# Kernel tuning notes

Hardware: AMD Instinct MI355X
Metric: run time of the kernel (lower is better)

## Reference

```python
import jax, jax.numpy as jnp
import numpy as np

H = W = 224
NOISE_STD = 0.45
BRIGHTNESS = 1.1          # uniform(0.8, 1.2) in original
ANGLE_DEG = 10.0          # randint(-20, 21) in original
CROP_I, CROP_J, CROP_SZ = 32, 32, 160

# Perspective: startpoints (input corners) -> endpoints (output corners).
STARTPOINTS = [[0, 0], [223, 0], [223, 223], [0, 223]]
ENDPOINTS = [[30, 20], [200, 25], [210, 200], [15, 190]]  # fixed draws within original ranges

def _perspective_coeffs(startpoints, endpoints):
    # Solve homography mapping OUTPUT coords (endpoints) -> INPUT coords (startpoints),
    # same convention as torchvision._get_perspective_coeffs(endpoints, startpoints).
    A = np.zeros((8, 8), dtype=np.float64)
    b = np.zeros((8,), dtype=np.float64)
    for k, ((xi, yi), (xo, yo)) in enumerate(zip(startpoints, endpoints)):
        A[2 * k] = [xo, yo, 1, 0, 0, 0, -xo * xi, -yo * xi]
        b[2 * k] = xi
        A[2 * k + 1] = [0, 0, 0, xo, yo, 1, -xo * yi, -yo * yi]
        b[2 * k + 1] = yi
    return np.linalg.solve(A, b)  # a,b,c,d,e,f,g,h

COEFFS = _perspective_coeffs(STARTPOINTS, ENDPOINTS)

def bilinear_sample(img, src_x, src_y):
    # img: [B,C,H,W]; src_x/src_y: [Ho,Wo] source pixel coords; zero fill outside.
    Hh, Ww = img.shape[-2], img.shape[-1]
    x0 = jnp.floor(src_x); y0 = jnp.floor(src_y)
    wx1 = src_x - x0; wx0 = 1.0 - wx1
    wy1 = src_y - y0; wy0 = 1.0 - wy1
    def gather(yi, xi):
        valid = (xi >= 0) & (xi <= Ww - 1) & (yi >= 0) & (yi <= Hh - 1)
        xc = jnp.clip(xi, 0, Ww - 1).astype(jnp.int32)
        yc = jnp.clip(yi, 0, Hh - 1).astype(jnp.int32)
        return img[:, :, yc, xc] * valid.astype(img.dtype)
    return (gather(y0, x0) * (wy0 * wx0) + gather(y0, x0 + 1) * (wy0 * wx1)
            + gather(y0 + 1, x0) * (wy1 * wx0) + gather(y0 + 1, x0 + 1) * (wy1 * wx1))

def perspective_grid():
    a, b_, c, d, e, f, g, h = [float(v) for v in COEFFS]
    yo, xo = jnp.meshgrid(jnp.arange(H, dtype=jnp.float32), jnp.arange(W, dtype=jnp.float32), indexing='ij')
    denom = g * xo + h * yo + 1.0
    return (a * xo + b_ * yo + c) / denom, (d * xo + e * yo + f) / denom

def rotate_grid(angle_deg):
    cx, cy = (W - 1) / 2.0, (H - 1) / 2.0
    t = jnp.float32(np.deg2rad(angle_deg))
    cos, sin = jnp.cos(t), jnp.sin(t)
    yo, xo = jnp.meshgrid(jnp.arange(H, dtype=jnp.float32), jnp.arange(W, dtype=jnp.float32), indexing='ij')
    dx, dy = xo - cx, yo - cy
    return cx + cos * dx + sin * dy, cy - sin * dx + cos * dy

def setup_inputs() -> dict:
    key = jax.random.key(0)
    k1, k2 = jax.random.split(key)
    x = jax.random.uniform(k1, (128, 3, H, W), dtype=jnp.float32)
    noise = jax.random.normal(k2, (128, 3, H, W), dtype=jnp.float32)
    return {"x": x, "noise": noise}

def reference(x, noise):
    # (hflip result discarded in the original -> no-op)
    x = x + NOISE_STD * noise                       # additive gaussian noise
    x = jnp.clip(x * BRIGHTNESS, 0.0, 1.0)          # adjust_brightness (float clamp to [0,1])
    px, py = perspective_grid()
    x = bilinear_sample(x, px, py)                  # perspective warp, bilinear, fill 0
    rx, ry = rotate_grid(ANGLE_DEG)
    x = bilinear_sample(x, rx, ry)                  # rotate, bilinear, fill 0
    x = x[..., CROP_I:CROP_I + CROP_SZ, CROP_J:CROP_J + CROP_SZ]  # 160x160 crop
    B, C = x.shape[0], x.shape[1]
    x = jax.image.resize(x, (B, C, H, W), method='bicubic')       # bicubic upsample back to 224
    return x
```

## Files before the change

kernel.cpp:

```cpp
#include <hip/hip_runtime.h>
#include <cmath>
#include <cstring>

#define HH 224
#define WW 224
#define CROP 160
#define CI 32
#define CJ 32
#define NCH 384
#define CH_STRIDE (HH*WW)
#define CROP_STRIDE (CROP*CROP)

#define TILE2 32
#define NTIL2 5
#define GCH2 8
#define BH2 64
#define BHCAP 62
#define NG2 18
#define BWSTR 80

#define TILE 16
#define NTIL 10
#define GCH 8
#define BMAXH 33
#define BMAXW 35
#define LROWS 35
#define LSTR  37
#define LWORDS (LROWS*LSTR)

struct AugParams {
  float a, b, c, d, e, f, g, h;
  float cosT, sinT;
};

__device__ __forceinline__ void axis_weights(int o, float w[4], int id[4]) {
  float s = (o + 0.5f) * (160.0f / 224.0f) - 0.5f;
  int base = (int)floorf(s) - 1;
  float sum = 0.0f;
#pragma unroll
  for (int t = 0; t < 4; ++t) {
    int ii = base + t;
    float dd = fabsf(s - (float)ii);
    float kw;
    if (dd < 1.0f)      kw = ((1.5f * dd - 2.5f) * dd) * dd + 1.0f;
    else if (dd < 2.0f) kw = ((-0.5f * dd + 2.5f) * dd - 4.0f) * dd + 2.0f;
    else                kw = 0.0f;
    if (ii < 0 || ii > CROP - 1) kw = 0.0f;
    w[t] = kw;
    sum += kw;
    id[t] = min(max(ii, 0), CROP - 1);
  }
  float inv = 1.0f / sum;
#pragma unroll
  for (int t = 0; t < 4; ++t) w[t] *= inv;
}

__global__ void table_kernel(float4* __restrict__ wt, int4* __restrict__ it) {
  int o = blockIdx.x * blockDim.x + threadIdx.x;
  if (o >= HH) return;
  float w[4]; int id[4];
  axis_weights(o, w, id);
  wt[o] = make_float4(w[0], w[1], w[2], w[3]);
  it[o] = make_int4(id[0], id[1], id[2], id[3]);
}

__device__ __forceinline__ float preproc(float v, float nv) {
  float p = (v + 0.45f * nv) * 1.1f;
  return fminf(fmaxf(p, 0.0f), 1.0f);
}

__device__ __forceinline__ float bf2f(unsigned short u) {
  return __uint_as_float(((unsigned int)u) << 16);
}

__device__ __forceinline__ unsigned short f2bf(float f) {
  unsigned int b = __float_as_uint(f);
  return (unsigned short)((b + 0x7fff + ((b >> 16) & 1)) >> 16);
}

__global__ __launch_bounds__(256) void preproc_kernel(
    const float4* __restrict__ xin, const float4* __restrict__ nin,
    ushort4* __restrict__ pre) {
  int t = blockIdx.x * 256 + threadIdx.x;
  int b = t * 4;
  float4 x0 = xin[b + 0], x1 = xin[b + 1], x2 = xin[b + 2], x3 = xin[b + 3];
  float4 n0 = nin[b + 0], n1 = nin[b + 1], n2 = nin[b + 2], n3 = nin[b + 3];
  ushort4 o0, o1, o2, o3;
  o0.x = f2bf(preproc(x0.x, n0.x)); o0.y = f2bf(preproc(x0.y, n0.y));
  o0.z = f2bf(preproc(x0.z, n0.z)); o0.w = f2bf(preproc(x0.w, n0.w));
  o1.x = f2bf(preproc(x1.x, n1.x)); o1.y = f2bf(preproc(x1.y, n1.y));
  o1.z = f2bf(preproc(x1.z, n1.z)); o1.w = f2bf(preproc(x1.w, n1.w));
  o2.x = f2bf(preproc(x2.x, n2.x)); o2.y = f2bf(preproc(x2.y, n2.y));
  o2.z = f2bf(preproc(x2.z, n2.z)); o2.w = f2bf(preproc(x2.w, n2.w));
  o3.x = f2bf(preproc(x3.x, n3.x)); o3.y = f2bf(preproc(x3.y, n3.y));
  o3.z = f2bf(preproc(x3.z, n3.z)); o3.w = f2bf(preproc(x3.w, n3.w));
  pre[b + 0] = o0; pre[b + 1] = o1; pre[b + 2] = o2; pre[b + 3] = o3;
}

__device__ __forceinline__ void make_taps(int i, int j, const AugParams P,
                                          int txs[16], int tys[16], float wts[16]) {
  const float cx = (WW - 1) * 0.5f, cy = (HH - 1) * 0.5f;
  float xr = (float)(j + CJ), yr = (float)(i + CI);
  float dx = xr - cx, dy = yr - cy;
  float rx = cx + P.cosT * dx + P.sinT * dy;
  float ry = cy - P.sinT * dx + P.cosT * dy;
  float x0f = floorf(rx), y0f = floorf(ry);
  int x0 = (int)x0f, y0 = (int)y0f;
  float wx1 = rx - x0f, wy1 = ry - y0f;
  float rwx[2] = {1.0f - wx1, wx1};
  float rwy[2] = {1.0f - wy1, wy1};
  int k = 0;
#pragma unroll
  for (int ny = 0; ny < 2; ++ny) {
#pragma unroll
    for (int nx = 0; nx < 2; ++nx) {
      int yn = y0 + ny, xn = x0 + nx;
      bool vn = (xn >= 0 && xn <= WW - 1 && yn >= 0 && yn <= HH - 1);
      float wn = rwy[ny] * rwx[nx] * (vn ? 1.0f : 0.0f);
      float xo = (float)xn, yo = (float)yn;
      float inv = 1.0f / (P.g * xo + P.h * yo + 1.0f);
      float px = (P.a * xo + P.b * yo + P.c) * inv;
      float py = (P.d * xo + P.e * yo + P.f) * inv;
      float px0f = floorf(px), py0f = floorf(py);
      int px0 = (int)px0f, py0 = (int)py0f;
      float pwx1 = px - px0f, pwy1 = py - py0f;
      float pwx[2] = {1.0f - pwx1, pwx1};
      float pwy[2] = {1.0f - pwy1, pwy1};
#pragma unroll
      for (int ty = 0; ty < 2; ++ty) {
#pragma unroll
        for (int tx = 0; tx < 2; ++tx) {
          int yt = py0 + ty, xt = px0 + tx;
          bool vt = (xt >= 0 && xt <= WW - 1 && yt >= 0 && yt <= HH - 1);
          tys[k] = min(max(yt, 0), HH - 1);
          txs[k] = min(max(xt, 0), WW - 1);
          wts[k] = wn * pwy[ty] * pwx[tx] * (vt ? 1.0f : 0.0f);
          ++k;
        }
      }
    }
  }
}

__device__ __forceinline__ void make_patches2(int i, int j, const AugParams P,
                                              int by0, int bx0e,
                                              int pofs[4], float wts[16]) {
  const float cx = (WW - 1) * 0.5f, cy = (HH - 1) * 0.5f;
  float xr = (float)(j + CJ), yr = (float)(i + CI);
  float dx = xr - cx, dy = yr - cy;
  float rx = cx + P.cosT * dx + P.sinT * dy;
  float ry = cy - P.sinT * dx + P.cosT * dy;
  float x0f = floorf(rx), y0f = floorf(ry);
  int x0 = (int)x0f, y0 = (int)y0f;
  float wx1 = rx - x0f, wy1 = ry - y0f;
  float rwx[2] = {1.0f - wx1, wx1};
  float rwy[2] = {1.0f - wy1, wy1};
  int n = 0;
#pragma unroll
  for (int ny = 0; ny < 2; ++ny) {
#pragma unroll
    for (int nx = 0; nx < 2; ++nx) {
      int yn = y0 + ny, xn = x0 + nx;
      bool vn = (xn >= 0 && xn <= WW - 1 && yn >= 0 && yn <= HH - 1);
      float wn = rwy[ny] * rwx[nx] * (vn ? 1.0f : 0.0f);
      float xo = (float)xn, yo = (float)yn;
      float inv = 1.0f / (P.g * xo + P.h * yo + 1.0f);
      float px = (P.a * xo + P.b * yo + P.c) * inv;
      float py = (P.d * xo + P.e * yo + P.f) * inv;
      float px0f = floorf(px), py0f = floorf(py);
      int px0 = (int)px0f, py0 = (int)py0f;
      float pwx1 = px - px0f, pwy1 = py - py0f;
      float pwx[2] = {1.0f - pwx1, pwx1};
      float pwy[2] = {1.0f - pwy1, pwy1};
#pragma unroll
      for (int ty = 0; ty < 2; ++ty) {
#pragma unroll
        for (int tx = 0; tx < 2; ++tx) {
          int yt = py0 + ty, xt = px0 + tx;
          bool vt = (xt >= 0 && xt <= WW - 1 && yt >= 0 && yt <= HH - 1);
          wts[n * 4 + ty * 2 + tx] = wn * pwy[ty] * pwx[tx] * (vt ? 1.0f : 0.0f);
        }
      }
      int r0 = py0 - by0 + 1;
      int c0 = px0 - bx0e + 4;
      r0 = min(max(r0, 0), BH2 - 2);
      c0 = min(max(c0, 0), BWSTR - 2);
      pofs[n] = r0 * BWSTR + c0;
      ++n;
    }
  }
}

__global__ __launch_bounds__(256, 3) void warp_pre_kernel(
    const unsigned short* __restrict__ pre, float* __restrict__ crop,
    AugParams P) {
  __shared__ float s_img[2][BH2 * BWSTR];
  int tile = blockIdx.x;
  int ch0  = blockIdx.y * GCH2;
  int i0 = (tile / NTIL2) * TILE2;
  int j0 = (tile % NTIL2) * TILE2;

  const float cx = (WW - 1) * 0.5f, cy = (HH - 1) * 0.5f;
  float rxmin = 1e30f, rxmax = -1e30f, rymin = 1e30f, rymax = -1e30f;
#pragma unroll
  for (int c = 0; c < 4; ++c) {
    float xr = (float)(j0 + CJ + ((c & 1) ? TILE2 - 1 : 0));
    float yr = (float)(i0 + CI + ((c & 2) ? TILE2 - 1 : 0));
    float dx = xr - cx, dy = yr - cy;
    float rx = cx + P.cosT * dx + P.sinT * dy;
    float ry = cy - P.sinT * dx + P.cosT * dy;
    rxmin = fminf(rxmin, rx); rxmax = fmaxf(rxmax, rx);
    rymin = fminf(rymin, ry); rymax = fmaxf(rymax, ry);
  }
  float xnlo = floorf(rxmin), xnhi = floorf(rxmax) + 1.0f;
  float ynlo = floorf(rymin), ynhi = floorf(rymax) + 1.0f;
  float pxmin = 1e30f, pxmax = -1e30f, pymin = 1e30f, pymax = -1e30f;
#pragma unroll
  for (int c = 0; c < 4; ++c) {
    float xo = (c & 1) ? xnhi : xnlo;
    float yo = (c & 2) ? ynhi : ynlo;
    float inv = 1.0f / (P.g * xo + P.h * yo + 1.0f);
    float px = (P.a * xo + P.b * yo + P.c) * inv;
    float py = (P.d * xo + P.e * yo + P.f) * inv;
    pxmin = fminf(pxmin, px); pxmax = fmaxf(pxmax, px);
    pymin = fminf(pymin, py); pymax = fmaxf(pymax, py);
  }
  int bx0 = max(0, (int)floorf(pxmin));
  int bx1 = min(WW - 1, (int)floorf(pxmax) + 1);
  int by0 = max(0, (int)floorf(pymin));
  int by1 = min(HH - 1, (int)floorf(pymax) + 1);
  int bx0e = bx0 & ~3;
  int bh = by1 - by0 + 1;
  int gmax = (bx1 - bx0e + 4) >> 2;
  bool use_lds = (bh <= BHCAP) && (gmax <= NG2 - 1);

  int tid = threadIdx.x;

  if (use_lds) {
    int pofs[4][4]; float wts[4][16];
#pragma unroll
    for (int k = 0; k < 4; ++k) {
      int p = tid + k * 256;
      make_patches2(i0 + (p >> 5), j0 + (p & 31), P, by0, bx0e, pofs[k], wts[k]);
    }

    for (int s = tid; s < 2 * BH2 * BWSTR; s += 256)
      ((float*)s_img)[s] = 0.0f;
    __syncthreads();

    int nslots = bh * NG2;
    {
      const unsigned short* pb = pre + (size_t)ch0 * CH_STRIDE;
#pragma unroll
      for (int q = 0; q < 5; ++q) {
        int s = tid + q * 256;
        if (s < nslots) {
          int r = s / NG2, g = s - r * NG2;
          int x = bx0e - 4 + g * 4;
          if (x >= 0 && g <= gmax) {
            ushort4 v = *(const ushort4*)(pb + (by0 + r) * WW + x);
            *(float4*)&s_img[0][(r + 1) * BWSTR + g * 4] =
                make_float4(bf2f(v.x), bf2f(v.y), bf2f(v.z), bf2f(v.w));
          }
        }
      }
      __syncthreads();
    }

    int buf = 0;
    for (int cc = 0; cc < GCH2; ++cc) {
      int ch = ch0 + cc;
      bool more = (cc < GCH2 - 1);
      ushort4 xv[5];
      if (more) {
        const unsigned short* pb = pre + (size_t)(ch + 1) * CH_STRIDE;
#pragma unroll
        for (int q = 0; q < 5; ++q) {
          int s = tid + q * 256;
          if (s < nslots) {
            int r = s / NG2, g = s - r * NG2;
            int x = bx0e - 4 + g * 4;
            if (x >= 0 && g <= gmax)
              xv[q] = *(const ushort4*)(pb + (by0 + r) * WW + x);
          }
        }
      }
      const float* sb = s_img[buf];
      float* cb = crop + (size_t)ch * CROP_STRIDE;
#pragma unroll
      for (int k = 0; k < 4; ++k) {
        int p = tid + k * 256;
        float acc = 0.0f;
#pragma unroll
        for (int n = 0; n < 4; ++n) {
          int o = pofs[k][n];
          float v00 = sb[o],         v01 = sb[o + 1];
          float v10 = sb[o + BWSTR], v11 = sb[o + BWSTR + 1];
          acc = fmaf(wts[k][n * 4 + 0], v00, acc);
          acc = fmaf(wts[k][n * 4 + 1], v01, acc);
          acc = fmaf(wts[k][n * 4 + 2], v10, acc);
          acc = fmaf(wts[k][n * 4 + 3], v11, acc);
        }
        cb[i0 * CROP + (p >> 5) * CROP + j0 + (p & 31)] = acc;
      }
      if (more) {
        float* sw = s_img[buf ^ 1];
#pragma unroll
        for (int q = 0; q < 5; ++q) {
          int s = tid + q * 256;
          if (s < nslots) {
            int r = s / NG2, g = s - r * NG2;
            int x = bx0e - 4 + g * 4;
            if (x >= 0 && g <= gmax) {
              *(float4*)&sw[(r + 1) * BWSTR + g * 4] =
                  make_float4(bf2f(xv[q].x), bf2f(xv[q].y),
                              bf2f(xv[q].z), bf2f(xv[q].w));
            }
          }
        }
      }
      __syncthreads();
      buf ^= 1;
    }
  } else {
    for (int k = 0; k < 4; ++k) {
      int p = tid + k * 256;
      int i = i0 + (p >> 5), j = j0 + (p & 31);
      int txs[16], tys[16]; float w[16];
      make_taps(i, j, P, txs, tys, w);
      for (int cc = 0; cc < GCH2; ++cc) {
        int ch = ch0 + cc;
        const unsigned short* pb = pre + (size_t)ch * CH_STRIDE;
        float acc = 0.0f;
#pragma unroll
        for (int t = 0; t < 16; ++t)
          acc = fmaf(w[t], bf2f(pb[tys[t] * WW + txs[t]]), acc);
        crop[(size_t)ch * CROP_STRIDE + i * CROP + j] = acc;
      }
    }
  }
}

__device__ __forceinline__ void make_patches(int i, int j, const AugParams P,
                                             int by0, int bx0, int bh, int bw,
                                             int pofs[4], float wts[16]) {
  const float cx = (WW - 1) * 0.5f, cy = (HH - 1) * 0.5f;
  float xr = (float)(j + CJ), yr = (float)(i + CI);
  float dx = xr - cx, dy = yr - cy;
  float rx = cx + P.cosT * dx + P.sinT * dy;
  float ry = cy - P.sinT * dx + P.cosT * dy;
  float x0f = floorf(rx), y0f = floorf(ry);
  int x0 = (int)x0f, y0 = (int)y0f;
  float wx1 = rx - x0f, wy1 = ry - y0f;
  float rwx[2] = {1.0f - wx1, wx1};
  float rwy[2] = {1.0f - wy1, wy1};
  int n = 0;
#pragma unroll
  for (int ny = 0; ny < 2; ++ny) {
#pragma unroll
    for (int nx = 0; nx < 2; ++nx) {
      int yn = y0 + ny, xn = x0 + nx;
      bool vn = (xn >= 0 && xn <= WW - 1 && yn >= 0 && yn <= HH - 1);
      float wn = rwy[ny] * rwx[nx] * (vn ? 1.0f : 0.0f);
      float xo = (float)xn, yo = (float)yn;
      float inv = 1.0f / (P.g * xo + P.h * yo + 1.0f);
      float px = (P.a * xo + P.b * yo + P.c) * inv;
      float py = (P.d * xo + P.e * yo + P.f) * inv;
      float px0f = floorf(px), py0f = floorf(py);
      int px0 = (int)px0f, py0 = (int)py0f;
      float pwx1 = px - px0f, pwy1 = py - py0f;
      float pwx[2] = {1.0f - pwx1, pwx1};
      float pwy[2] = {1.0f - pwy1, pwy1};
#pragma unroll
      for (int ty = 0; ty < 2; ++ty) {
#pragma unroll
        for (int tx = 0; tx < 2; ++tx) {
          int yt = py0 + ty, xt = px0 + tx;
          bool vt = (xt >= 0 && xt <= WW - 1 && yt >= 0 && yt <= HH - 1);
          wts[n * 4 + ty * 2 + tx] = wn * pwy[ty] * pwx[tx] * (vt ? 1.0f : 0.0f);
        }
      }
      int ly = py0 - by0;
      int lx = px0 - bx0;
      if (ly < -1 || ly > bh - 1) ly = 0;
      if (lx < -1 || lx > bw - 1) lx = 0;
      pofs[n] = (ly + 1) * LSTR + (lx + 1);
      ++n;
    }
  }
}

__global__ __launch_bounds__(256) void warp_direct_kernel(
    const float* __restrict__ xin, const float* __restrict__ nin,
    float* __restrict__ crop, AugParams P) {
  __shared__ float s_img[2][LWORDS];
  int tile = blockIdx.x;
  int ch0  = blockIdx.y * GCH;
  int i0 = (tile / NTIL) * TILE;
  int j0 = (tile % NTIL) * TILE;

  const float cx = (WW - 1) * 0.5f, cy = (HH - 1) * 0.5f;
  float rxmin = 1e30f, rxmax = -1e30f, rymin = 1e30f, rymax = -1e30f;
#pragma unroll
  for (int c = 0; c < 4; ++c) {
    float xr = (float)(j0 + CJ + ((c & 1) ? TILE - 1 : 0));
    float yr = (float)(i0 + CI + ((c & 2) ? TILE - 1 : 0));
    float dx = xr - cx, dy = yr - cy;
    float rx = cx + P.cosT * dx + P.sinT * dy;
    float ry = cy - P.sinT * dx + P.cosT * dy;
    rxmin = fminf(rxmin, rx); rxmax = fmaxf(rxmax, rx);
    rymin = fminf(rymin, ry); rymax = fmaxf(rymax, ry);
  }
  float xnlo = floorf(rxmin), xnhi = floorf(rxmax) + 1.0f;
  float ynlo = floorf(rymin), ynhi = floorf(rymax) + 1.0f;
  float pxmin = 1e30f, pxmax = -1e30f, pymin = 1e30f, pymax = -1e30f;
#pragma unroll
  for (int c = 0; c < 4; ++c) {
    float xo = (c & 1) ? xnhi : xnlo;
    float yo = (c & 2) ? ynhi : ynlo;
    float inv = 1.0f / (P.g * xo + P.h * yo + 1.0f);
    float px = (P.a * xo + P.b * yo + P.c) * inv;
    float py = (P.d * xo + P.e * yo + P.f) * inv;
    pxmin = fminf(pxmin, px); pxmax = fmaxf(pxmax, px);
    pymin = fminf(pymin, py); pymax = fmaxf(pymax, py);
  }
  int bx0 = max(0, (int)floorf(pxmin));
  int bx1 = min(WW - 1, (int)floorf(pxmax) + 1);
  int by0 = max(0, (int)floorf(pymin));
  int by1 = min(HH - 1, (int)floorf(pymax) + 1);
  int bw = bx1 - bx0 + 1;
  int bh = by1 - by0 + 1;
  bool use_lds = (bw <= BMAXW && bh <= BMAXH);

  int tid = threadIdx.x;
  int i = i0 + (tid >> 4);
  int j = j0 + (tid & 15);
  int opix = i * CROP + j;

  if (use_lds) {
    int pofs[4]; float wts[16];
    make_patches(i, j, P, by0, bx0, bh, bw, pofs, wts);
    for (int s = tid; s < 2 * LWORDS; s += 256)
      ((float*)s_img)[s] = 0.0f;
    __syncthreads();
    {
      const float* xb = xin + (size_t)ch0 * CH_STRIDE;
      const float* nb = nin + (size_t)ch0 * CH_STRIDE;
      int r = tid >> 5, c = tid & 31;
#pragma unroll
      for (int rr = 0; rr < 5; ++rr) {
        int rcur = r + rr * 8;
        if (rcur < bh && c < bw) {
          int g = (by0 + rcur) * WW + bx0 + c;
          s_img[0][(rcur + 1) * LSTR + (c + 1)] = preproc(xb[g], nb[g]);
        }
      }
      if (bw > 32) {
        int r2 = tid >> 2, c2 = 32 + (tid & 3);
        if (r2 < bh && c2 < bw) {
          int g = (by0 + r2) * WW + bx0 + c2;
          s_img[0][(r2 + 1) * LSTR + (c2 + 1)] = preproc(xb[g], nb[g]);
        }
      }
      __syncthreads();
    }
    int buf = 0;
    int r = tid >> 5, c = tid & 31;
    int r2 = tid >> 2, c2 = 32 + (tid & 3);
    for (int cc = 0; cc < GCH; ++cc) {
      int ch = ch0 + cc;
      bool more = (cc < GCH - 1);
      float xv[5], nv[5], xe = 0.0f, ne = 0.0f;
      if (more) {
        const float* xb = xin + (size_t)(ch + 1) * CH_STRIDE;
        const float* nb = nin + (size_t)(ch + 1) * CH_STRIDE;
#pragma unroll
        for (int rr = 0; rr < 5; ++rr) {
          int rcur = r + rr * 8;
          if (rcur < bh && c < bw) {
            int g = (by0 + rcur) * WW + bx0 + c;
            xv[rr] = xb[g]; nv[rr] = nb[g];
          }
        }
        if (bw > 32 && r2 < bh && c2 < bw) {
          int g = (by0 + r2) * WW + bx0 + c2;
          xe = xb[g]; ne = nb[g];
        }
      }
      const float* sb = s_img[buf];
      float acc = 0.0f;
#pragma unroll
      for (int n = 0; n < 4; ++n) {
        int p = pofs[n];
        acc = fmaf(wts[n * 4 + 0], sb[p], acc);
        acc = fmaf(wts[n * 4 + 1], sb[p + 1], acc);
        acc = fmaf(wts[n * 4 + 2], sb[p + LSTR], acc);
        acc = fmaf(wts[n * 4 + 3], sb[p + LSTR + 1], acc);
      }
      crop[(size_t)ch * CROP_STRIDE + opix] = acc;
      if (more) {
        float* sw = s_img[buf ^ 1];
#pragma unroll
        for (int rr = 0; rr < 5; ++rr) {
          int rcur = r + rr * 8;
          if (rcur < bh && c < bw)
            sw[(rcur + 1) * LSTR + (c + 1)] = preproc(xv[rr], nv[rr]);
        }
        if (bw > 32 && r2 < bh && c2 < bw)
          sw[(r2 + 1) * LSTR + (c2 + 1)] = preproc(xe, ne);
      }
      __syncthreads();
      buf ^= 1;
    }
  } else {
    int txs[16], tys[16]; float wts[16];
    make_taps(i, j, P, txs, tys, wts);
    for (int cc = 0; cc < GCH; ++cc) {
      int ch = ch0 + cc;
      const float* xb = xin + (size_t)ch * CH_STRIDE;
      const float* nb = nin + (size_t)ch * CH_STRIDE;
      float acc = 0.0f;
#pragma unroll
      for (int t = 0; t < 16; ++t) {
        int g = tys[t] * WW + txs[t];
        acc = fmaf(wts[t], preproc(xb[g], nb[g]), acc);
      }
      crop[(size_t)ch * CROP_STRIDE + opix] = acc;
    }
  }
}

#define STRIPROWS 28
#define HROWS 25
__global__ __launch_bounds__(256) void resize_strips_kernel(
    const float* __restrict__ crop, const float4* __restrict__ wt,
    const int4* __restrict__ it, float* __restrict__ out) {
  __shared__ float hbuf[HROWS * WW];
  int s = blockIdx.x;
  int ch = blockIdx.y;
  int r0 = max(0, s * 20 - 2);
  const float* cb = crop + (size_t)ch * CROP_STRIDE;
  int tid = threadIdx.x;

  for (int e = tid; e < HROWS * WW; e += 256) {
    int r = e / WW;
    int xo = e - r * WW;
    int cr = min(r0 + r, CROP - 1);
    float4 wx = wt[xo]; int4 ix = it[xo];
    const float* row = cb + cr * CROP;
    hbuf[e] = wx.x * row[ix.x] + wx.y * row[ix.y] +
              wx.z * row[ix.z] + wx.w * row[ix.w];
  }
  __syncthreads();
  for (int e = tid; e < STRIPROWS * WW; e += 256) {
    int yl = e / WW;
    int xo = e - yl * WW;
    int yo = s * STRIPROWS + yl;
    float4 wy = wt[yo]; int4 iy = it[yo];
    float o = wy.x * hbuf[(iy.x - r0) * WW + xo] +
              wy.y * hbuf[(iy.y - r0) * WW + xo] +
              wy.z * hbuf[(iy.z - r0) * WW + xo] +
              wy.w * hbuf[(iy.w - r0) * WW + xo];
    __builtin_nontemporal_store(o, &out[((size_t)ch * HH + yo) * WW + xo]);
  }
}

__device__ float crop_val(const float* __restrict__ xb, const float* __restrict__ nb,
                          int i, int j, AugParams P) {
  int txs[16], tys[16]; float wts[16];
  make_taps(i, j, P, txs, tys, wts);
  float acc = 0.0f;
#pragma unroll
  for (int t = 0; t < 16; ++t)
    acc = fmaf(wts[t], preproc(xb[tys[t] * WW + txs[t]], nb[tys[t] * WW + txs[t]]), acc);
  return acc;
}

__global__ __launch_bounds__(256) void fused_fallback_kernel(
    const float* __restrict__ xin, const float* __restrict__ nin,
    float* __restrict__ out, AugParams P, int total) {
  int stride = gridDim.x * blockDim.x;
  for (int idx = blockIdx.x * blockDim.x + threadIdx.x; idx < total; idx += stride) {
    int xo = idx % WW;
    int t2 = idx / WW;
    int yo = t2 % HH;
    int ch = t2 / HH;
    float wxa[4]; int ixa[4]; axis_weights(xo, wxa, ixa);
    float wya[4]; int iya[4]; axis_weights(yo, wya, iya);
    const float* xb = xin + (size_t)ch * CH_STRIDE;
    const float* nb = nin + (size_t)ch * CH_STRIDE;
    float acc = 0.0f;
#pragma unroll
    for (int ty = 0; ty < 4; ++ty)
#pragma unroll
      for (int tx = 0; tx < 4; ++tx)
        acc += wya[ty] * wxa[tx] * crop_val(xb, nb, iya[ty], ixa[tx], P);
    out[idx] = acc;
  }
}

static void solve_coeffs(double C[8]) {
  const double sp[4][2] = {{0, 0}, {223, 0}, {223, 223}, {0, 223}};
  const double ep[4][2] = {{30, 20}, {200, 25}, {210, 200}, {15, 190}};
  double A[8][9];
  for (int k = 0; k < 4; ++k) {
    double xi = sp[k][0], yi = sp[k][1], xo = ep[k][0], yo = ep[k][1];
    double r0[9] = {xo, yo, 1, 0, 0, 0, -xo * xi, -yo * xi, xi};
    double r1[9] = {0, 0, 0, xo, yo, 1, -xo * yi, -yo * yi, yi};
    std::memcpy(A[2 * k], r0, sizeof r0);
    std::memcpy(A[2 * k + 1], r1, sizeof r1);
  }
  for (int col = 0; col < 8; ++col) {
    int piv = col;
    for (int r = col + 1; r < 8; ++r)
      if (std::fabs(A[r][col]) > std::fabs(A[piv][col])) piv = r;
    if (piv != col)
      for (int cc = 0; cc < 9; ++cc) { double t = A[col][cc]; A[col][cc] = A[piv][cc]; A[piv][cc] = t; }
    double p = A[col][col];
    for (int r = 0; r < 8; ++r) {
      if (r == col) continue;
      double fmul = A[r][col] / p;
      for (int cc = col; cc < 9; ++cc) A[r][cc] -= fmul * A[col][cc];
    }
  }
  for (int r = 0; r < 8; ++r) C[r] = A[r][8] / A[r][r];
}

extern "C" void kernel_launch(void* const* d_in, const int* in_sizes, int n_in,
                              void* d_out, int out_size, void* d_ws, size_t ws_size,
                              hipStream_t stream) {
  const float* xin = (const float*)d_in[0];
  const float* nin = (const float*)d_in[1];
  float* out = (float*)d_out;

  double C[8];
  solve_coeffs(C);
  AugParams P;
  P.a = (float)C[0]; P.b = (float)C[1]; P.c = (float)C[2]; P.d = (float)C[3];
  P.e = (float)C[4]; P.f = (float)C[5]; P.g = (float)C[6]; P.h = (float)C[7];
  double t = 10.0 * M_PI / 180.0;
  P.cosT = (float)std::cos(t);
  P.sinT = (float)std::sin(t);

  const int total = NCH * HH * WW;
  const size_t PRE_BYTES = (size_t)NCH * CH_STRIDE * 2;
  const size_t CROP_BYTES = (size_t)NCH * CROP_STRIDE * 4;

  const size_t TBLW_OFF = PRE_BYTES + 256;
  const size_t TBLI_OFF = TBLW_OFF + 3584;
  const size_t CROPF_OFF = TBLI_OFF + 3584;
  const size_t need_full = CROPF_OFF + CROP_BYTES;
  const size_t need_med = 8192 + CROP_BYTES;

  if (ws_size >= need_full) {
    unsigned short* pre = (unsigned short*)d_ws;
    float4* wt = (float4*)((char*)d_ws + TBLW_OFF);
    int4*   it = (int4*)((char*)d_ws + TBLI_OFF);
    float* crop = (float*)((char*)d_ws + CROPF_OFF);

    hipLaunchKernelGGL(table_kernel, dim3(1), dim3(256), 0, stream, wt, it);
    hipLaunchKernelGGL(preproc_kernel, dim3(total / 16 / 256), dim3(256), 0, stream,
                       (const float4*)xin, (const float4*)nin, (ushort4*)pre);
    dim3 g1(NTIL2 * NTIL2, NCH / GCH2);
    hipLaunchKernelGGL(warp_pre_kernel, g1, dim3(256), 0, stream, pre, crop, P);
    dim3 g2(HH / STRIPROWS, NCH);
    hipLaunchKernelGGL(resize_strips_kernel, g2, dim3(256), 0, stream, crop, wt, it, out);
  } else if (ws_size >= need_med) {
    float4* wt = (float4*)d_ws;
    int4*   it = (int4*)((char*)d_ws + 3584);
    float* crop = (float*)((char*)d_ws + 8192);

    hipLaunchKernelGGL(table_kernel, dim3(1), dim3(256), 0, stream, wt, it);
    dim3 g1(NTIL * NTIL, NCH / GCH);
    hipLaunchKernelGGL(warp_direct_kernel, g1, dim3(256), 0, stream, xin, nin, crop, P);
    dim3 g2(HH / STRIPROWS, NCH);
    hipLaunchKernelGGL(resize_strips_kernel, g2, dim3(256), 0, stream, crop, wt, it, out);
  } else {
    hipLaunchKernelGGL(fused_fallback_kernel, dim3(2048), dim3(256), 0, stream,
                       xin, nin, out, P, total);
  }
}
```

Baseline: 121.0 us.

## Shrink warp LDS tile, swizzle blocks across XCDs, inline resize tables, widen preproc

Several independent changes. The warp kernel's LDS tile shrinks from 64x80 to 46x56 floats so occupancy can rise from 3 to 4 blocks per CU, and it gains a right-edge bound check. The warp and preproc kernels remap block IDs so neighbouring blocks spread across the 8 XCDs. The separate table kernel is removed, and each resize block recomputes its bicubic weights into shared memory, which drops one launch but repeats a little work in every block. Preproc now writes ushort8 vectors, with its loads separated from the conversion by a scheduling barrier. The smaller tile fits fewer source rows, so more tiles may fall back to the slower non-LDS path.

```diff
diff --git a/kernel.cpp b/kernel.cpp
--- a/kernel.cpp
+++ b/kernel.cpp
@@ -14,10 +14,10 @@
 #define TILE2 32
 #define NTIL2 5
 #define GCH2 8
-#define BH2 64
-#define BHCAP 62
-#define NG2 18
-#define BWSTR 80
+#define BROWS 46
+#define BHCAP 44
+#define NG2 14
+#define BSTR 56
 
 #define TILE 16
 #define NTIL 10
@@ -27,6 +27,8 @@
 #define LROWS 35
 #define LSTR  37
 #define LWORDS (LROWS*LSTR)
+
+typedef unsigned short ushort8 __attribute__((ext_vector_type(8)));
 
 struct AugParams {
   float a, b, c, d, e, f, g, h;
@@ -55,15 +57,6 @@
   for (int t = 0; t < 4; ++t) w[t] *= inv;
 }
 
-__global__ void table_kernel(float4* __restrict__ wt, int4* __restrict__ it) {
-  int o = blockIdx.x * blockDim.x + threadIdx.x;
-  if (o >= HH) return;
-  float w[4]; int id[4];
-  axis_weights(o, w, id);
-  wt[o] = make_float4(w[0], w[1], w[2], w[3]);
-  it[o] = make_int4(id[0], id[1], id[2], id[3]);
-}
-
 __device__ __forceinline__ float preproc(float v, float nv) {
   float p = (v + 0.45f * nv) * 1.1f;
   return fminf(fmaxf(p, 0.0f), 1.0f);
@@ -80,21 +73,27 @@
 
 __global__ __launch_bounds__(256) void preproc_kernel(
     const float4* __restrict__ xin, const float4* __restrict__ nin,
-    ushort4* __restrict__ pre) {
-  int t = blockIdx.x * 256 + threadIdx.x;
-  int b = t * 4;
-  float4 x0 = xin[b + 0], x1 = xin[b + 1], x2 = xin[b + 2], x3 = xin[b + 3];
-  float4 n0 = nin[b + 0], n1 = nin[b + 1], n2 = nin[b + 2], n3 = nin[b + 3];
-  ushort4 o0, o1, o2, o3;
-  o0.x = f2bf(preproc(x0.x, n0.x)); o0.y = f2bf(preproc(x0.y, n0.y));
-  o0.z = f2bf(preproc(x0.z, n0.z)); o0.w = f2bf(preproc(x0.w, n0.w));
-  o1.x = f2bf(preproc(x1.x, n1.x)); o1.y = f2bf(preproc(x1.y, n1.y));
-  o1.z = f2bf(preproc(x1.z, n1.z)); o1.w = f2bf(preproc(x1.w, n1.w));
-  o2.x = f2bf(preproc(x2.x, n2.x)); o2.y = f2bf(preproc(x2.y, n2.y));
-  o2.z = f2bf(preproc(x2.z, n2.z)); o2.w = f2bf(preproc(x2.w, n2.w));
-  o3.x = f2bf(preproc(x3.x, n3.x)); o3.y = f2bf(preproc(x3.y, n3.y));
-  o3.z = f2bf(preproc(x3.z, n3.z)); o3.w = f2bf(preproc(x3.w, n3.w));
-  pre[b + 0] = o0; pre[b + 1] = o1; pre[b + 2] = o2; pre[b + 3] = o3;
+    ushort8* __restrict__ pre) {
+  int blk = blockIdx.x;
+  blk = (blk & 7) * 588 + (blk >> 3);
+  int g0 = blk * 512 + threadIdx.x;
+  int g1 = g0 + 256;
+  float4 xa = xin[2 * g0], xb = xin[2 * g0 + 1];
+  float4 xc = xin[2 * g1], xd = xin[2 * g1 + 1];
+  float4 na = nin[2 * g0], nb = nin[2 * g0 + 1];
+  float4 nc = nin[2 * g1], nd = nin[2 * g1 + 1];
+  __builtin_amdgcn_sched_barrier(0);
+  ushort8 oa, ob;
+  oa[0] = f2bf(preproc(xa.x, na.x)); oa[1] = f2bf(preproc(xa.y, na.y));
+  oa[2] = f2bf(preproc(xa.z, na.z)); oa[3] = f2bf(preproc(xa.w, na.w));
+  oa[4] = f2bf(preproc(xb.x, nb.x)); oa[5] = f2bf(preproc(xb.y, nb.y));
+  oa[6] = f2bf(preproc(xb.z, nb.z)); oa[7] = f2bf(preproc(xb.w, nb.w));
+  ob[0] = f2bf(preproc(xc.x, nc.x)); ob[1] = f2bf(preproc(xc.y, nc.y));
+  ob[2] = f2bf(preproc(xc.z, nc.z)); ob[3] = f2bf(preproc(xc.w, nc.w));
+  ob[4] = f2bf(preproc(xd.x, nd.x)); ob[5] = f2bf(preproc(xd.y, nd.y));
+  ob[6] = f2bf(preproc(xd.z, nd.z)); ob[7] = f2bf(preproc(xd.w, nd.w));
+  pre[g0] = oa;
+  pre[g1] = ob;
 }
 
 __device__ __forceinline__ void make_taps(int i, int j, const AugParams P,
@@ -183,20 +182,22 @@
       }
       int r0 = py0 - by0 + 1;
       int c0 = px0 - bx0e + 4;
-      r0 = min(max(r0, 0), BH2 - 2);
-      c0 = min(max(c0, 0), BWSTR - 2);
-      pofs[n] = r0 * BWSTR + c0;
+      r0 = min(max(r0, 0), BROWS - 2);
+      c0 = min(max(c0, 0), BSTR - 2);
+      pofs[n] = r0 * BSTR + c0;
       ++n;
     }
   }
 }
 
-__global__ __launch_bounds__(256, 3) void warp_pre_kernel(
+__global__ __launch_bounds__(256, 4) void warp_pre_kernel(
     const unsigned short* __restrict__ pre, float* __restrict__ crop,
     AugParams P) {
-  __shared__ float s_img[2][BH2 * BWSTR];
-  int tile = blockIdx.x;
-  int ch0  = blockIdx.y * GCH2;
+  __shared__ float s_img[2][BROWS * BSTR];
+  int lb = blockIdx.x + blockIdx.y * (NTIL2 * NTIL2);
+  lb = (lb & 7) * 150 + (lb >> 3);
+  int tile = lb % (NTIL2 * NTIL2);
+  int ch0  = (lb / (NTIL2 * NTIL2)) * GCH2;
   int i0 = (tile / NTIL2) * TILE2;
   int j0 = (tile % NTIL2) * TILE2;
 
@@ -244,7 +245,7 @@
       make_patches2(i0 + (p >> 5), j0 + (p & 31), P, by0, bx0e, pofs[k], wts[k]);
     }
 
-    for (int s = tid; s < 2 * BH2 * BWSTR; s += 256)
+    for (int s = tid; s < 2 * BROWS * BSTR; s += 256)
       ((float*)s_img)[s] = 0.0f;
     __syncthreads();
 
@@ -252,14 +253,14 @@
     {
       const unsigned short* pb = pre + (size_t)ch0 * CH_STRIDE;
 #pragma unroll
-      for (int q = 0; q < 5; ++q) {
+      for (int q = 0; q < 3; ++q) {
         int s = tid + q * 256;
         if (s < nslots) {
           int r = s / NG2, g = s - r * NG2;
           int x = bx0e - 4 + g * 4;
-          if (x >= 0 && g <= gmax) {
+          if (x >= 0 && x <= WW - 4 && g <= gmax) {
             ushort4 v = *(const ushort4*)(pb + (by0 + r) * WW + x);
-            *(float4*)&s_img[0][(r + 1) * BWSTR + g * 4] =
+            *(float4*)&s_img[0][(r + 1) * BSTR + g * 4] =
                 make_float4(bf2f(v.x), bf2f(v.y), bf2f(v.z), bf2f(v.w));
           }
         }
@@ -271,16 +272,16 @@
     for (int cc = 0; cc < GCH2; ++cc) {
       int ch = ch0 + cc;
       bool more = (cc < GCH2 - 1);
-      ushort4 xv[5];
+      ushort4 xv[3];
       if (more) {
         const unsigned short* pb = pre + (size_t)(ch + 1) * CH_STRIDE;
 #pragma unroll
-        for (int q = 0; q < 5; ++q) {
+        for (int q = 0; q < 3; ++q) {
           int s = tid + q * 256;
           if (s < nslots) {
             int r = s / NG2, g = s - r * NG2;
             int x = bx0e - 4 + g * 4;
-            if (x >= 0 && g <= gmax)
+            if (x >= 0 && x <= WW - 4 && g <= gmax)
               xv[q] = *(const ushort4*)(pb + (by0 + r) * WW + x);
           }
         }
@@ -294,8 +295,8 @@
 #pragma unroll
         for (int n = 0; n < 4; ++n) {
           int o = pofs[k][n];
-          float v00 = sb[o],         v01 = sb[o + 1];
-          float v10 = sb[o + BWSTR], v11 = sb[o + BWSTR + 1];
+          float v00 = sb[o],        v01 = sb[o + 1];
+          float v10 = sb[o + BSTR], v11 = sb[o + BSTR + 1];
           acc = fmaf(wts[k][n * 4 + 0], v00, acc);
           acc = fmaf(wts[k][n * 4 + 1], v01, acc);
           acc = fmaf(wts[k][n * 4 + 2], v10, acc);
@@ -306,13 +307,13 @@
       if (more) {
         float* sw = s_img[buf ^ 1];
 #pragma unroll
-        for (int q = 0; q < 5; ++q) {
+        for (int q = 0; q < 3; ++q) {
           int s = tid + q * 256;
           if (s < nslots) {
             int r = s / NG2, g = s - r * NG2;
             int x = bx0e - 4 + g * 4;
-            if (x >= 0 && g <= gmax) {
-              *(float4*)&sw[(r + 1) * BWSTR + g * 4] =
+            if (x >= 0 && x <= WW - 4 && g <= gmax) {
+              *(float4*)&sw[(r + 1) * BSTR + g * 4] =
                   make_float4(bf2f(xv[q].x), bf2f(xv[q].y),
                               bf2f(xv[q].z), bf2f(xv[q].w));
             }
@@ -533,20 +534,29 @@
 #define STRIPROWS 28
 #define HROWS 25
 __global__ __launch_bounds__(256) void resize_strips_kernel(
-    const float* __restrict__ crop, const float4* __restrict__ wt,
-    const int4* __restrict__ it, float* __restrict__ out) {
+    const float* __restrict__ crop, float* __restrict__ out) {
   __shared__ float hbuf[HROWS * WW];
+  __shared__ float4 swt[HH];
+  __shared__ int4 sit[HH];
   int s = blockIdx.x;
   int ch = blockIdx.y;
   int r0 = max(0, s * 20 - 2);
   const float* cb = crop + (size_t)ch * CROP_STRIDE;
   int tid = threadIdx.x;
 
+  if (tid < HH) {
+    float w[4]; int id[4];
+    axis_weights(tid, w, id);
+    swt[tid] = make_float4(w[0], w[1], w[2], w[3]);
+    sit[tid] = make_int4(id[0], id[1], id[2], id[3]);
+  }
+  __syncthreads();
+
   for (int e = tid; e < HROWS * WW; e += 256) {
     int r = e / WW;
     int xo = e - r * WW;
     int cr = min(r0 + r, CROP - 1);
-    float4 wx = wt[xo]; int4 ix = it[xo];
+    float4 wx = swt[xo]; int4 ix = sit[xo];
     const float* row = cb + cr * CROP;
     hbuf[e] = wx.x * row[ix.x] + wx.y * row[ix.y] +
               wx.z * row[ix.z] + wx.w * row[ix.w];
@@ -556,7 +566,7 @@
     int yl = e / WW;
     int xo = e - yl * WW;
     int yo = s * STRIPROWS + yl;
-    float4 wy = wt[yo]; int4 iy = it[yo];
+    float4 wy = swt[yo]; int4 iy = sit[yo];
     float o = wy.x * hbuf[(iy.x - r0) * WW + xo] +
               wy.y * hbuf[(iy.y - r0) * WW + xo] +
               wy.z * hbuf[(iy.z - r0) * WW + xo] +
@@ -645,36 +655,26 @@
   const int total = NCH * HH * WW;
   const size_t PRE_BYTES = (size_t)NCH * CH_STRIDE * 2;
   const size_t CROP_BYTES = (size_t)NCH * CROP_STRIDE * 4;
-
-  const size_t TBLW_OFF = PRE_BYTES + 256;
-  const size_t TBLI_OFF = TBLW_OFF + 3584;
-  const size_t CROPF_OFF = TBLI_OFF + 3584;
-  const size_t need_full = CROPF_OFF + CROP_BYTES;
-  const size_t need_med = 8192 + CROP_BYTES;
+  const size_t need_full = PRE_BYTES + CROP_BYTES;
+  const size_t need_med = CROP_BYTES;
 
   if (ws_size >= need_full) {
     unsigned short* pre = (unsigned short*)d_ws;
-    float4* wt = (float4*)((char*)d_ws + TBLW_OFF);
-    int4*   it = (int4*)((char*)d_ws + TBLI_OFF);
-    float* crop = (float*)((char*)d_ws + CROPF_OFF);
-
-    hipLaunchKernelGGL(table_kernel, dim3(1), dim3(256), 0, stream, wt, it);
-    hipLaunchKernelGGL(preproc_kernel, dim3(total / 16 / 256), dim3(256), 0, stream,
-                       (const float4*)xin, (const float4*)nin, (ushort4*)pre);
+    float* crop = (float*)((char*)d_ws + PRE_BYTES);
+
+    hipLaunchKernelGGL(preproc_kernel, dim3(4704), dim3(256), 0, stream,
+                       (const float4*)xin, (const float4*)nin, (ushort8*)pre);
     dim3 g1(NTIL2 * NTIL2, NCH / GCH2);
     hipLaunchKernelGGL(warp_pre_kernel, g1, dim3(256), 0, stream, pre, crop, P);
     dim3 g2(HH / STRIPROWS, NCH);
-    hipLaunchKernelGGL(resize_strips_kernel, g2, dim3(256), 0, stream, crop, wt, it, out);
+    hipLaunchKernelGGL(resize_strips_kernel, g2, dim3(256), 0, stream, crop, out);
   } else if (ws_size >= need_med) {
-    float4* wt = (float4*)d_ws;
-    int4*   it = (int4*)((char*)d_ws + 3584);
-    float* crop = (float*)((char*)d_ws + 8192);
-
-    hipLaunchKernelGGL(table_kernel, dim3(1), dim3(256), 0, stream, wt, it);
+    float* crop = (float*)d_ws;
+
     dim3 g1(NTIL * NTIL, NCH / GCH);
     hipLaunchKernelGGL(warp_direct_kernel, g1, dim3(256), 0, stream, xin, nin, crop, P);
     dim3 g2(HH / STRIPROWS, NCH);
-    hipLaunchKernelGGL(resize_strips_kernel, g2, dim3(256), 0, stream, crop, wt, it, out);
+    hipLaunchKernelGGL(resize_strips_kernel, g2, dim3(256), 0, stream, crop, out);
   } else {
     hipLaunchKernelGGL(fused_fallback_kernel, dim3(2048), dim3(256), 0, stream,
                        xin, nin, out, P, total);
```

Result: slower. 219.1 us (+81.1%).
